# Kernel tuning notes

Measured on AMD Instinct MI355X. Metric: run time of the kernel, lower is better.

## Reference

```python
import jax, jax.numpy as jnp
import numpy as np

LN_EPS = 1e-5


def _layernorm_2d(x, w, b):
    # LayerNorm over the last two dims (d, d) with elementwise affine.
    mu = jnp.mean(x, axis=(-2, -1), keepdims=True)
    var = jnp.var(x, axis=(-2, -1), keepdims=True)
    return (x - mu) * jax.lax.rsqrt(var + LN_EPS) * w + b


def setup_inputs() -> dict:
    key = jax.random.key(0)
    k_x, k_a, k_w, k_b = jax.random.split(key, 4)
    B, T, D = 2, 512, 64
    x = jax.random.normal(k_x, (B, T, D, D), dtype=jnp.float32)
    log_A = jax.random.normal(k_a, (D,), dtype=jnp.float32) * 0.02
    # dt_proj: nn.Linear(dim, 1) -> weight (1, dim) stored here as (dim,), bias (1,)
    bound = 1.0 / np.sqrt(D)
    dt_w = jax.random.uniform(k_w, (D,), dtype=jnp.float32, minval=-bound, maxval=bound)
    dt_b = jax.random.uniform(k_b, (1,), dtype=jnp.float32, minval=-bound, maxval=bound)
    ln_w = jnp.ones((D, D), dtype=jnp.float32)
    ln_b = jnp.zeros((D, D), dtype=jnp.float32)
    return {"x": x, "log_A": log_A, "dt_w": dt_w, "dt_b": dt_b, "ln_w": ln_w, "ln_b": ln_b}


def reference(x, log_A, dt_w, dt_b, ln_w, ln_b):
    B, T, D, _ = x.shape
    xn = _layernorm_2d(x, ln_w, ln_b)                          # [B,T,D,D]
    A_cont = -jnp.exp(log_A)                                   # [D]
    dt = jax.nn.softplus(jnp.einsum('btrc,c->btr', xn, dt_w) + dt_b)  # [B,T,D]
    log_decay = dt * A_cont                                    # [B,T,D]
    cs = jnp.cumsum(log_decay, axis=1)                         # [B,T,D]
    log_M = cs[:, :, None, :] - cs[:, None, :, :]              # [B,T,T,D]
    idx = jnp.arange(T)
    causal = (idx[:, None] >= idx[None, :])[None, :, :, None]  # [1,T,T,1]
    M = jnp.exp(jnp.where(causal, log_M, -jnp.inf))            # [B,T,T,D]
    out = jnp.einsum('btjr,bjrc->btrc', M, xn)                 # [B,T,D,D]
    return out
```

## Files before the change

### kernel.cpp

```cpp
#include <hip/hip_runtime.h>
#include <math.h>

#define B_SZ 2
#define T_SZ 512
#define D_SZ 64
#define ELEMS 4096
#define NW2 8
#define TCH 64

#define DECAY_BYTES ((size_t)B_SZ * D_SZ * T_SZ * 4)
#define STATS_OFF   DECAY_BYTES

__global__ __launch_bounds__(256) void ln_dt_kernel(
    const float* __restrict__ x, const float* __restrict__ log_A,
    const float* __restrict__ dt_w, const float* __restrict__ dt_b,
    const float* __restrict__ ln_w, const float* __restrict__ ln_b,
    float* __restrict__ decay_t, float2* __restrict__ stats)
{
    const int bt  = blockIdx.x;
    const int tid = threadIdx.x;
    const size_t base = (size_t)bt * ELEMS;

    float4 v[4];
    float sum = 0.f, sumsq = 0.f;
    const float4* xv4 = reinterpret_cast<const float4*>(x + base);
#pragma unroll
    for (int k = 0; k < 4; ++k) {
        v[k] = xv4[tid + 256 * k];
        sum   += v[k].x + v[k].y + v[k].z + v[k].w;
        sumsq += v[k].x * v[k].x + v[k].y * v[k].y + v[k].z * v[k].z + v[k].w * v[k].w;
    }

    __shared__ float red0[4], red1[4];
#pragma unroll
    for (int off = 32; off; off >>= 1) {
        sum   += __shfl_down(sum, off);
        sumsq += __shfl_down(sumsq, off);
    }
    const int wave = tid >> 6;
    if ((tid & 63) == 0) { red0[wave] = sum; red1[wave] = sumsq; }
    __syncthreads();
    sum   = red0[0] + red0[1] + red0[2] + red0[3];
    sumsq = red1[0] + red1[1] + red1[2] + red1[3];

    const float mu = sum * (1.f / ELEMS);
    const float var = sumsq * (1.f / ELEMS) - mu * mu;
    const float rs = rsqrtf(var + 1e-5f);

    const float4* w4p = reinterpret_cast<const float4*>(ln_w);
    const float4* b4p = reinterpret_cast<const float4*>(ln_b);
    const float4* dw4 = reinterpret_cast<const float4*>(dt_w);
    float dot[4] = {0.f, 0.f, 0.f, 0.f};
#pragma unroll
    for (int k = 0; k < 4; ++k) {
        const int f = tid + 256 * k;
        float4 w4 = w4p[f];
        float4 b4 = b4p[f];
        float4 xn;
        xn.x = (v[k].x - mu) * rs * w4.x + b4.x;
        xn.y = (v[k].y - mu) * rs * w4.y + b4.y;
        xn.z = (v[k].z - mu) * rs * w4.z + b4.z;
        xn.w = (v[k].w - mu) * rs * w4.w + b4.w;
        float4 wv = dw4[f & 15];
        dot[k] += xn.x * wv.x + xn.y * wv.y + xn.z * wv.z + xn.w * wv.w;
    }

#pragma unroll
    for (int m = 1; m <= 8; m <<= 1) {
#pragma unroll
        for (int k = 0; k < 4; ++k) dot[k] += __shfl_xor(dot[k], m);
    }

    if (tid == 0) stats[bt] = make_float2(mu, rs);

    if ((tid & 15) == 0) {
        const int m = tid >> 4;
        const float db = dt_b[0];
        const int b = bt >> 9;
        const int t = bt & (T_SZ - 1);
#pragma unroll
        for (int k = 0; k < 4; ++k) {
            const int r = m + 16 * k;
            const float z = dot[k] + db;
            const float dt = (z > 20.f) ? z : log1pf(expf(z));
            const float A = -expf(log_A[r]);
            decay_t[((size_t)(b * D_SZ + r)) * T_SZ + t] = expf(dt * A);
        }
    }
}

__global__ __launch_bounds__(NW2 * 64) void scan_fused_kernel(
    const float* __restrict__ x, const float2* __restrict__ stats,
    const float* __restrict__ decay_t,
    const float* __restrict__ ln_w, const float* __restrict__ ln_b,
    float* __restrict__ out)
{
    const int tid  = threadIdx.x;
    const int lane = tid & 63;
    const int w    = tid >> 6;
    const int row  = blockIdx.x;
    const int b = row >> 6;
    const int r = row & 63;

    __shared__ float  sd[T_SZ];
    __shared__ float2 sst[T_SZ];
    __shared__ float  sS[NW2][64];
    __shared__ float  sP[NW2];

    if (tid < T_SZ) {
        sd[tid]  = decay_t[(size_t)row * T_SZ + tid];
        sst[tid] = stats[(size_t)b * T_SZ + tid];
    }
    const float wr = ln_w[r * D_SZ + lane];
    const float br = ln_b[r * D_SZ + lane];
    __syncthreads();

    const int t0 = w * TCH;
    const float* xp = x + ((size_t)(b * T_SZ + t0) * D_SZ + r) * D_SZ + lane;

    float v[TCH];
    float S = 0.f;
#pragma unroll
    for (int i = 0; i < TCH; ++i) {
        const float  xv = xp[(size_t)i * ELEMS];
        const float2 st = sst[t0 + i];
        const float  xn = fmaf((xv - st.x) * st.y, wr, br);
        S = fmaf(S, sd[t0 + i], xn);
        v[i] = S;
    }

    float P = 1.f;
#pragma unroll
    for (int i = 0; i < TCH; ++i) P *= sd[t0 + i];

    sS[w][lane] = S;
    if (lane == 0) sP[w] = P;
    __syncthreads();

    float Cin = 0.f;
    for (int j = 0; j < w; ++j)
        Cin = fmaf(sP[j], Cin, sS[j][lane]);

    float* op = out + ((size_t)(b * T_SZ + t0) * D_SZ + r) * D_SZ + lane;
    float rp = 1.f;
#pragma unroll
    for (int i = 0; i < TCH; ++i) {
        rp *= sd[t0 + i];
        op[(size_t)i * ELEMS] = fmaf(rp, Cin, v[i]);
    }
}

extern "C" void kernel_launch(void* const* d_in, const int* in_sizes, int n_in,
                              void* d_out, int out_size, void* d_ws, size_t ws_size,
                              hipStream_t stream) {
    const float* x     = (const float*)d_in[0];
    const float* log_A = (const float*)d_in[1];
    const float* dt_w  = (const float*)d_in[2];
    const float* dt_b  = (const float*)d_in[3];
    const float* ln_w  = (const float*)d_in[4];
    const float* ln_b  = (const float*)d_in[5];
    float* out     = (float*)d_out;
    float* decay_t = (float*)d_ws;
    float2* stats  = (float2*)((char*)d_ws + STATS_OFF);

    ln_dt_kernel<<<B_SZ * T_SZ, 256, 0, stream>>>(
        x, log_A, dt_w, dt_b, ln_w, ln_b, decay_t, stats);

    scan_fused_kernel<<<B_SZ * D_SZ, NW2 * 64, 0, stream>>>(
        x, stats, decay_t, ln_w, ln_b, out);
}
```

Measured before the change: 24.09 us.

## Split scan into four column-quarter blocks with shorter 16-step chunks

```diff
diff --git a/kernel.cpp b/kernel.cpp
--- a/kernel.cpp
+++ b/kernel.cpp
@@ -5,8 +5,10 @@
 #define T_SZ 512
 #define D_SZ 64
 #define ELEMS 4096
-#define NW2 8
-#define TCH 64
+
+#define NCH  32
+#define CLEN 16
+#define NCOL 16
 
 #define DECAY_BYTES ((size_t)B_SZ * D_SZ * T_SZ * 4)
 #define STATS_OFF   DECAY_BYTES
@@ -89,39 +91,41 @@
     }
 }
 
-__global__ __launch_bounds__(NW2 * 64) void scan_fused_kernel(
+__global__ __launch_bounds__(512, 4) void scan_fused_kernel(
     const float* __restrict__ x, const float2* __restrict__ stats,
     const float* __restrict__ decay_t,
     const float* __restrict__ ln_w, const float* __restrict__ ln_b,
     float* __restrict__ out)
 {
-    const int tid  = threadIdx.x;
-    const int lane = tid & 63;
-    const int w    = tid >> 6;
-    const int row  = blockIdx.x;
+    const int tid = threadIdx.x;
+    const int col = tid & (NCOL - 1);
+    const int k   = tid >> 4;
+    const int row = blockIdx.x >> 2;
+    const int cq  = blockIdx.x & 3;
     const int b = row >> 6;
     const int r = row & 63;
+    const int c = cq * NCOL + col;
 
     __shared__ float  sd[T_SZ];
     __shared__ float2 sst[T_SZ];
-    __shared__ float  sS[NW2][64];
-    __shared__ float  sP[NW2];
+    __shared__ float  sS[NCH][NCOL];
+    __shared__ float  sP[NCH];
 
     if (tid < T_SZ) {
         sd[tid]  = decay_t[(size_t)row * T_SZ + tid];
         sst[tid] = stats[(size_t)b * T_SZ + tid];
     }
-    const float wr = ln_w[r * D_SZ + lane];
-    const float br = ln_b[r * D_SZ + lane];
+    const float wr = ln_w[r * D_SZ + c];
+    const float br = ln_b[r * D_SZ + c];
     __syncthreads();
 
-    const int t0 = w * TCH;
-    const float* xp = x + ((size_t)(b * T_SZ + t0) * D_SZ + r) * D_SZ + lane;
+    const int t0 = k * CLEN;
+    const float* xp = x + ((size_t)(b * T_SZ + t0) * D_SZ + r) * D_SZ + c;
 
-    float v[TCH];
+    float v[CLEN];
     float S = 0.f;
 #pragma unroll
-    for (int i = 0; i < TCH; ++i) {
+    for (int i = 0; i < CLEN; ++i) {
         const float  xv = xp[(size_t)i * ELEMS];
         const float2 st = sst[t0 + i];
         const float  xn = fmaf((xv - st.x) * st.y, wr, br);
@@ -129,22 +133,23 @@
         v[i] = S;
     }
 
-    float P = 1.f;
+    if (col == 0) {
+        float P = 1.f;
 #pragma unroll
-    for (int i = 0; i < TCH; ++i) P *= sd[t0 + i];
-
-    sS[w][lane] = S;
-    if (lane == 0) sP[w] = P;
+        for (int i = 0; i < CLEN; ++i) P *= sd[t0 + i];
+        sP[k] = P;
+    }
+    sS[k][col] = S;
     __syncthreads();
 
     float Cin = 0.f;
-    for (int j = 0; j < w; ++j)
-        Cin = fmaf(sP[j], Cin, sS[j][lane]);
+    for (int j = 0; j < k; ++j)
+        Cin = fmaf(sP[j], Cin, sS[j][col]);
 
-    float* op = out + ((size_t)(b * T_SZ + t0) * D_SZ + r) * D_SZ + lane;
+    float* op = out + ((size_t)(b * T_SZ + t0) * D_SZ + r) * D_SZ + c;
     float rp = 1.f;
 #pragma unroll
-    for (int i = 0; i < TCH; ++i) {
+    for (int i = 0; i < CLEN; ++i) {
         rp *= sd[t0 + i];
         op[(size_t)i * ELEMS] = fmaf(rp, Cin, v[i]);
     }
@@ -166,6 +171,6 @@
     ln_dt_kernel<<<B_SZ * T_SZ, 256, 0, stream>>>(
         x, log_A, dt_w, dt_b, ln_w, ln_b, decay_t, stats);
 
-    scan_fused_kernel<<<B_SZ * D_SZ, NW2 * 64, 0, stream>>>(
+    scan_fused_kernel<<<B_SZ * D_SZ * 4, 512, 0, stream>>>(
         x, stats, decay_t, ln_w, ln_b, out);
 }
```

Measured after the change: 25.46 us. +5.7%, slower.
